# Performance work log

Measured on AMD Instinct MI355X. Metric: run time of the kernel, lower is better.

## Reference

```python
import jax, jax.numpy as jnp
import numpy as np

H, DH = 16, 32  # hardcoded by E's shape [16, seq, 32]


def setup_inputs() -> dict:
    key = jax.random.key(0)
    k1, k2 = jax.random.split(key)
    B, S = 2, 2048
    x = jax.random.normal(k1, (B, S, 3 * H * DH), dtype=jnp.float32)
    E = jax.random.normal(k2, (H, S, DH), dtype=jnp.float32) * 0.02  # learned rel-pos table
    return {"x": x, "E": E}


def _skew(rel):
    # Music-Transformer skew trick: rel [B,H,S,S] -> relative-position alignment.
    B, Hh, S, _ = rel.shape
    rel = jnp.pad(rel, ((0, 0), (0, 0), (0, 0), (1, 0)))  # pad left on last dim
    rel = rel.reshape(B, Hh, S + 1, S)[:, :, 1:]
    return rel


def reference(x, E):
    B, S, _ = x.shape
    q, k, v = jnp.split(x, 3, axis=2)

    def heads(t):
        return t.reshape(B, S, H, DH).transpose(0, 2, 1, 3)  # [B,H,S,DH]

    q, k, v = heads(q), heads(k), heads(v)
    present = jnp.stack([k, v], axis=1)  # [B,2,H,S,DH]

    w = jnp.einsum('bhsd,bhtd->bhst', q, k)            # content scores
    rel = _skew(jnp.einsum('bhsd,hmd->bhsm', q, E))    # relative-position scores
    w = (w + rel) * jax.lax.rsqrt(jnp.float32(DH))     # scale AFTER adding rel (as in source)

    i = jnp.arange(S)[:, None]
    j = jnp.arange(S)[None, :]
    b = (i >= j).astype(w.dtype)                       # causal mask (nd == ns)
    w = w * b - jnp.float32(1e10) * (1.0 - b)
    w = jax.nn.softmax(w, axis=-1)

    a = jnp.einsum('bhst,bhtd->bhsd', w, v)
    a = a.transpose(0, 2, 1, 3).reshape(B, S, H * DH)  # merge heads -> [B,S,512]
    return a, present
```

## Files before the change

kernel.cpp:

```cpp
#include <hip/hip_runtime.h>
#include <hip/hip_bf16.h>

#define NH   16
#define DHD  32
#define SEQ  2048
#define NB   2
#define XROW 1536
#define PP   72

typedef unsigned short u16;
typedef __attribute__((ext_vector_type(8))) short bf16x8;
typedef __attribute__((ext_vector_type(4))) float f32x4;

static __device__ __forceinline__ u16 f2b(float f) {
    __hip_bfloat16 h = __float2bfloat16(f);
    return *(u16*)&h;
}

__global__ __launch_bounds__(256)
void prep_all(const float* __restrict__ x, const float* __restrict__ E,
              u16* __restrict__ Kb, u16* __restrict__ Vt, u16* __restrict__ Eb,
              float* __restrict__ pres) {
    __shared__ float t[64][33];
    int bid = blockIdx.x;
    int tid = threadIdx.x;
    if (bid < 1024) {
        long o = ((long)bid * 256 + tid) * 8;
        int d = (int)(o & 31);
        int s = (int)((o >> 5) & (SEQ - 1));
        int bh = (int)(o >> 16);
        int b = bh >> 4, h = bh & 15;
        const float* src = x + ((long)(b * SEQ + s)) * XROW + 512 + h * 32 + d;
        float4 f0 = *(const float4*)src, f1 = *(const float4*)(src + 4);
        u16 pk[8] = {f2b(f0.x), f2b(f0.y), f2b(f0.z), f2b(f0.w),
                     f2b(f1.x), f2b(f1.y), f2b(f1.z), f2b(f1.w)};
        *(uint4*)(Kb + o) = *(uint4*)pk;
    } else if (bid < 1536) {
        long o = ((long)(bid - 1024) * 256 + tid) * 8;
        const float* src = E + o;
        float4 f0 = *(const float4*)src, f1 = *(const float4*)(src + 4);
        u16 pk[8] = {f2b(f0.x), f2b(f0.y), f2b(f0.z), f2b(f0.w),
                     f2b(f1.x), f2b(f1.y), f2b(f1.z), f2b(f1.w)};
        *(uint4*)(Eb + o) = *(uint4*)pk;
    } else if (bid < 2560) {
        int vb = bid - 1536;
        int bh = vb & 31;
        int s0 = (vb >> 5) << 6;
        int b = bh >> 4, h = bh & 15;
        int sr = tid >> 3, d4 = (tid & 7) * 4;
        const float* base = x + (long)b * SEQ * XROW + 1024 + h * 32;
        float4 f = *(const float4*)(base + (long)(s0 + sr) * XROW + d4);
        t[sr][d4] = f.x; t[sr][d4+1] = f.y; t[sr][d4+2] = f.z; t[sr][d4+3] = f.w;
        f = *(const float4*)(base + (long)(s0 + sr + 32) * XROW + d4);
        t[sr+32][d4] = f.x; t[sr+32][d4+1] = f.y; t[sr+32][d4+2] = f.z; t[sr+32][d4+3] = f.w;
        __syncthreads();
        int d = tid >> 3, sg = (tid & 7) * 8;
        u16 pk[8];
#pragma unroll
        for (int k = 0; k < 8; ++k) pk[k] = f2b(t[sg + k][d]);
        *(uint4*)(Vt + ((long)(bh * 32 + d)) * SEQ + s0 + sg) = *(uint4*)pk;
    } else {
        long o = ((long)(bid - 2560) * 256 + tid) * 4;
        int d0 = (int)(o & 31);
        int s  = (int)((o >> 5) & (SEQ - 1));
        int h  = (int)((o >> 16) & (NH - 1));
        int c  = (int)((o >> 20) & 1);
        int b  = (int)(o >> 21);
        const float4* in = (const float4*)(x + ((long)(b * SEQ + s)) * XROW
                                           + (1 + c) * 512 + h * 32 + d0);
        *((float4*)(pres + o)) = in[0];
    }
}

__global__ __launch_bounds__(256, 8)
void attn_mfma(const float* __restrict__ x, const u16* __restrict__ Kb,
               const u16* __restrict__ Vt, const u16* __restrict__ Eb,
               float* __restrict__ out) {
    __shared__ u16  pls[4][16 * PP];
    __shared__ float comb[4][16][33];

    int bh = blockIdx.x & 31;
    int gt = 127 - (blockIdx.x >> 5);
    int b = bh >> 4, h = bh & 15;
    int wv   = threadIdx.x >> 6;
    int lane = threadIdx.x & 63;
    int n16  = lane & 15;
    int quad = lane >> 4;
    int i0 = gt * 16;

    const u16* Kbh = Kb + (long)bh * SEQ * 32;
    const u16* Vbh = Vt + (long)bh * 32 * SEQ;
    const u16* Ebh = Eb + (long)h * SEQ * 32;

    const float scale = 0.17677669529663687f;
    bf16x8 qf;
    {
        const float* qp = x + ((long)(b * SEQ) + i0 + n16) * XROW + h * 32 + quad * 8;
        float4 f0 = *(const float4*)qp, f1 = *(const float4*)(qp + 4);
        u16 pk[8] = {f2b(f0.x*scale), f2b(f0.y*scale), f2b(f0.z*scale), f2b(f0.w*scale),
                     f2b(f1.x*scale), f2b(f1.y*scale), f2b(f1.z*scale), f2b(f1.w*scale)};
        qf = *(bf16x8*)pk;
    }

    bf16x8 ones;
#pragma unroll
    for (int k = 0; k < 8; ++k) ones[k] = (short)0x3F80;

    f32x4 O0 = {0.f,0.f,0.f,0.f}, O1 = {0.f,0.f,0.f,0.f}, Os = {0.f,0.f,0.f,0.f};
    const f32x4 zero = {0.f,0.f,0.f,0.f};

    u16* pw = &pls[wv][0];
    int cbase = 15 - quad * 4 + n16;
    int permhi = (lane & 48) << 2;

    int nch = (i0 >> 6) + 1;
    for (int ch = wv; ch < nch; ch += 4) {
        int j0c = ch << 6;
        int mw0 = 2032 - i0 + j0c;

        f32x4 P0, P1;
        {
            int row = mw0 + n16; if (row > SEQ - 1) row = SEQ - 1;
            bf16x8 ef = *(const bf16x8*)(Ebh + (long)row * 32 + quad * 8);
            P0 = __builtin_amdgcn_mfma_f32_16x16x32_bf16(qf, ef, zero, 0, 0, 0);
        }
        f32x4 w[4];
#pragma unroll
        for (int s = 0; s < 4; ++s) {
            {
                int row = mw0 + 16 * (s + 1) + n16; if (row > SEQ - 1) row = SEQ - 1;
                bf16x8 ef = *(const bf16x8*)(Ebh + (long)row * 32 + quad * 8);
                P1 = __builtin_amdgcn_mfma_f32_16x16x32_bf16(qf, ef, zero, 0, 0, 0);
            }
            f32x4 C;
            {
                bf16x8 kf = *(const bf16x8*)(Kbh + (long)(j0c + 16*s + n16) * 32 + quad * 8);
                C = __builtin_amdgcn_mfma_f32_16x16x32_bf16(qf, kf, zero, 0, 0, 0);
            }
#pragma unroll
            for (int r = 0; r < 4; ++r) {
                int c = cbase - r;
                int addr = permhi | ((c & 15) << 2);
                int v0 = __builtin_amdgcn_ds_bpermute(addr, __float_as_int(P0[r]));
                int v1 = __builtin_amdgcn_ds_bpermute(addr, __float_as_int(P1[r]));
                float rel = (c < 16) ? __int_as_float(v0) : __int_as_float(v1);
                w[s][r] = C[r] + rel;
            }
            P0 = P1;
        }

        if (ch == nch - 1) {
            int jb = j0c + n16 - i0;
#pragma unroll
            for (int s = 0; s < 4; ++s)
#pragma unroll
                for (int r = 0; r < 4; ++r)
                    if (jb + 16 * s > quad * 4 + r) w[s][r] = -1e30f;
        }

#pragma unroll
        for (int s = 0; s < 4; ++s)
#pragma unroll
            for (int r = 0; r < 4; ++r)
                w[s][r] = __expf(w[s][r]);

#pragma unroll
        for (int s = 0; s < 4; ++s)
#pragma unroll
            for (int r = 0; r < 4; ++r)
                pw[(quad * 4 + r) * PP + 16 * s + n16] = f2b(w[s][r]);

        bf16x8 pa0 = *(const bf16x8*)(pw + n16 * PP + quad * 8);
        bf16x8 pa1 = *(const bf16x8*)(pw + n16 * PP + 32 + quad * 8);

        bf16x8 v00 = *(const bf16x8*)(Vbh + (long)n16 * SEQ        + j0c      + quad * 8);
        bf16x8 v01 = *(const bf16x8*)(Vbh + (long)n16 * SEQ        + j0c + 32 + quad * 8);
        bf16x8 v10 = *(const bf16x8*)(Vbh + (long)(16 + n16) * SEQ + j0c      + quad * 8);
        bf16x8 v11 = *(const bf16x8*)(Vbh + (long)(16 + n16) * SEQ + j0c + 32 + quad * 8);

        O0 = __builtin_amdgcn_mfma_f32_16x16x32_bf16(pa0, v00, O0, 0, 0, 0);
        O0 = __builtin_amdgcn_mfma_f32_16x16x32_bf16(pa1, v01, O0, 0, 0, 0);
        O1 = __builtin_amdgcn_mfma_f32_16x16x32_bf16(pa0, v10, O1, 0, 0, 0);
        O1 = __builtin_amdgcn_mfma_f32_16x16x32_bf16(pa1, v11, O1, 0, 0, 0);
        Os = __builtin_amdgcn_mfma_f32_16x16x32_bf16(pa0, ones, Os, 0, 0, 0);
        Os = __builtin_amdgcn_mfma_f32_16x16x32_bf16(pa1, ones, Os, 0, 0, 0);
    }

#pragma unroll
    for (int r = 0; r < 4; ++r) {
        comb[wv][quad * 4 + r][n16]      = O0[r];
        comb[wv][quad * 4 + r][16 + n16] = O1[r];
        if (n16 == 0) comb[wv][quad * 4 + r][32] = Os[r];
    }
    __syncthreads();

    int row = threadIdx.x >> 4;
    int c2  = (threadIdx.x & 15) * 2;
    float s0 = 0.f, s1 = 0.f, ls = 0.f;
#pragma unroll
    for (int v = 0; v < 4; ++v) {
        s0 += comb[v][row][c2];
        s1 += comb[v][row][c2 + 1];
        ls += comb[v][row][32];
    }
    float inv = 1.0f / ls;
    float* op = out + ((long)(b * SEQ) + i0 + row) * 512 + h * 32 + c2;
    op[0] = s0 * inv;
    op[1] = s1 * inv;
}

__global__ void present_copy(const float* __restrict__ x, float* __restrict__ pres) {
    long o = ((long)blockIdx.x * blockDim.x + threadIdx.x) * 4;
    int d0 = (int)(o & 31);
    int s  = (int)((o >> 5) & (SEQ - 1));
    int h  = (int)((o >> 16) & (NH - 1));
    int c  = (int)((o >> 20) & 1);
    int b  = (int)(o >> 21);
    const float4* in = (const float4*)(x + ((long)(b * SEQ + s)) * XROW
                                       + (1 + c) * 512 + h * 32 + d0);
    *((float4*)(pres + o)) = in[0];
}

__global__ __launch_bounds__(128)
void attn_mono(const float* __restrict__ x, const float* __restrict__ E,
               float* __restrict__ out) {
    __shared__ float kt[64][36];
    __shared__ float vt[64][36];
    __shared__ float et[192][33];
    int bh = blockIdx.x & 31;
    int rt = 15 - (blockIdx.x >> 5);
    int b = bh >> 4, h = bh & 15;
    int tid = threadIdx.x;
    int r0 = rt * 128;
    int i = r0 + tid;
    float q[DHD];
    const float4* q4 = (const float4*)(x + ((long)(b * SEQ + i)) * XROW + h * 32);
#pragma unroll
    for (int t = 0; t < 8; ++t) ((float4*)q)[t] = q4[t];
    float m = -1e30f, l = 0.f;
    float acc[DHD];
#pragma unroll
    for (int d = 0; d < DHD; ++d) acc[d] = 0.f;
    const float* Eh = E + (long)h * SEQ * DHD;
    int ntile = (rt + 1) * 2;
    for (int t0 = 0; t0 < ntile; ++t0) {
        int j0 = t0 * 64;
        {
            int r = tid & 63, isv = tid >> 6;
            const float4* s4 = (const float4*)(x + ((long)(b * SEQ + j0 + r)) * XROW
                                               + (1 + isv) * 512 + h * 32);
            float4 tmp[8];
#pragma unroll
            for (int t = 0; t < 8; ++t) tmp[t] = s4[t];
            float* dst = isv ? &vt[r][0] : &kt[r][0];
#pragma unroll
            for (int t = 0; t < 8; ++t) ((float4*)dst)[t] = tmp[t];
        }
        {
            int eb0 = (SEQ - 1) - (r0 + 127) + j0;
#pragma unroll
            for (int p = 0; p < 12; ++p) {
                int idx = p * 128 + tid;
                int r = idx >> 3, qq = idx & 7;
                int gr = eb0 + r; if (gr > SEQ - 1) gr = SEQ - 1;
                float4 gg = *(const float4*)(Eh + (long)gr * DHD + qq * 4);
                et[r][qq*4+0] = gg.x; et[r][qq*4+1] = gg.y;
                et[r][qq*4+2] = gg.z; et[r][qq*4+3] = gg.w;
            }
        }
        __syncthreads();
        int jend = i - j0 + 1; if (jend > 64) jend = 64;
        int er0 = 127 - tid;
        for (int jj = 0; jj < jend; ++jj) {
            const float* ep = &et[er0 + jj][0];
            float dk = 0.f, de = 0.f;
#pragma unroll
            for (int d = 0; d < DHD; ++d) {
                dk = __builtin_fmaf(q[d], kt[jj][d], dk);
                de = __builtin_fmaf(q[d], ep[d], de);
            }
            float sc = (dk + de) * 0.17677669529663687f;
            if (sc > m) {
                float r = __expf(m - sc);
                l *= r;
#pragma unroll
                for (int d = 0; d < DHD; ++d) acc[d] *= r;
                m = sc;
            }
            float p = __expf(sc - m);
            l += p;
#pragma unroll
            for (int d = 0; d < DHD; ++d)
                acc[d] = __builtin_fmaf(p, vt[jj][d], acc[d]);
        }
        __syncthreads();
    }
    float inv = 1.0f / l;
    float* op = out + ((long)(b * SEQ + i)) * 512 + h * 32;
#pragma unroll
    for (int t = 0; t < 8; ++t) {
        float4 w;
        w.x = acc[t*4+0]*inv; w.y = acc[t*4+1]*inv;
        w.z = acc[t*4+2]*inv; w.w = acc[t*4+3]*inv;
        ((float4*)op)[t] = w;
    }
}

extern "C" void kernel_launch(void* const* d_in, const int* in_sizes, int n_in,
                              void* d_out, int out_size, void* d_ws, size_t ws_size,
                              hipStream_t stream) {
    const float* x = (const float*)d_in[0];
    const float* E = (const float*)d_in[1];
    if (n_in >= 2 && in_sizes[0] == 1048576) { const float* t = x; x = E; E = t; }
    float* a    = (float*)d_out;
    float* pres = a + (long)NB * SEQ * NH * DHD;

    const long KN = (long)NB * NH * SEQ * 32;
    const long EN = (long)NH * SEQ * 32;
    const size_t WS_NEED = (size_t)(2 * KN + EN) * sizeof(u16);
    if (ws_size >= WS_NEED) {
        u16* Kb = (u16*)d_ws;
        u16* Vt = Kb + KN;
        u16* Eb = Vt + KN;
        prep_all<<<dim3(6656), dim3(256), 0, stream>>>(x, E, Kb, Vt, Eb, pres);
        attn_mfma<<<dim3(4096), dim3(256), 0, stream>>>(x, Kb, Vt, Eb, a);
    } else {
        attn_mono<<<dim3(512), dim3(128), 0, stream>>>(x, E, a);
        present_copy<<<dim3(4096), dim3(256), 0, stream>>>(x, pres);
    }
}
```

Before: 154.8 us.

## Fuse present copy into attention kernel and halve rel-pos bpermutes

```diff
diff --git a/kernel.cpp b/kernel.cpp
--- a/kernel.cpp
+++ b/kernel.cpp
@@ -19,8 +19,7 @@
 
 __global__ __launch_bounds__(256)
 void prep_all(const float* __restrict__ x, const float* __restrict__ E,
-              u16* __restrict__ Kb, u16* __restrict__ Vt, u16* __restrict__ Eb,
-              float* __restrict__ pres) {
+              u16* __restrict__ Kb, u16* __restrict__ Vt, u16* __restrict__ Eb) {
     __shared__ float t[64][33];
     int bid = blockIdx.x;
     int tid = threadIdx.x;
@@ -42,7 +41,7 @@
         u16 pk[8] = {f2b(f0.x), f2b(f0.y), f2b(f0.z), f2b(f0.w),
                      f2b(f1.x), f2b(f1.y), f2b(f1.z), f2b(f1.w)};
         *(uint4*)(Eb + o) = *(uint4*)pk;
-    } else if (bid < 2560) {
+    } else {
         int vb = bid - 1536;
         int bh = vb & 31;
         int s0 = (vb >> 5) << 6;
@@ -59,23 +58,13 @@
 #pragma unroll
         for (int k = 0; k < 8; ++k) pk[k] = f2b(t[sg + k][d]);
         *(uint4*)(Vt + ((long)(bh * 32 + d)) * SEQ + s0 + sg) = *(uint4*)pk;
-    } else {
-        long o = ((long)(bid - 2560) * 256 + tid) * 4;
-        int d0 = (int)(o & 31);
-        int s  = (int)((o >> 5) & (SEQ - 1));
-        int h  = (int)((o >> 16) & (NH - 1));
-        int c  = (int)((o >> 20) & 1);
-        int b  = (int)(o >> 21);
-        const float4* in = (const float4*)(x + ((long)(b * SEQ + s)) * XROW
-                                           + (1 + c) * 512 + h * 32 + d0);
-        *((float4*)(pres + o)) = in[0];
     }
 }
 
 __global__ __launch_bounds__(256, 8)
 void attn_mfma(const float* __restrict__ x, const u16* __restrict__ Kb,
                const u16* __restrict__ Vt, const u16* __restrict__ Eb,
-               float* __restrict__ out) {
+               float* __restrict__ out, float* __restrict__ pres) {
     __shared__ u16  pls[4][16 * PP];
     __shared__ float comb[4][16][33];
 
@@ -119,10 +108,17 @@
         int mw0 = 2032 - i0 + j0c;
 
         f32x4 P0, P1;
+        float rel0[4];
         {
             int row = mw0 + n16; if (row > SEQ - 1) row = SEQ - 1;
             bf16x8 ef = *(const bf16x8*)(Ebh + (long)row * 32 + quad * 8);
             P0 = __builtin_amdgcn_mfma_f32_16x16x32_bf16(qf, ef, zero, 0, 0, 0);
+        }
+#pragma unroll
+        for (int r = 0; r < 4; ++r) {
+            int addr = permhi | (((cbase - r) & 15) << 2);
+            rel0[r] = __int_as_float(
+                __builtin_amdgcn_ds_bpermute(addr, __float_as_int(P0[r])));
         }
         f32x4 w[4];
 #pragma unroll
@@ -141,10 +137,11 @@
             for (int r = 0; r < 4; ++r) {
                 int c = cbase - r;
                 int addr = permhi | ((c & 15) << 2);
-                int v0 = __builtin_amdgcn_ds_bpermute(addr, __float_as_int(P0[r]));
-                int v1 = __builtin_amdgcn_ds_bpermute(addr, __float_as_int(P1[r]));
-                float rel = (c < 16) ? __int_as_float(v0) : __int_as_float(v1);
+                float rel1 = __int_as_float(
+                    __builtin_amdgcn_ds_bpermute(addr, __float_as_int(P1[r])));
+                float rel = (c < 16) ? rel0[r] : rel1;
                 w[s][r] = C[r] + rel;
+                rel0[r] = rel1;
             }
             P0 = P1;
         }
@@ -207,6 +204,18 @@
     float* op = out + ((long)(b * SEQ) + i0 + row) * 512 + h * 32 + c2;
     op[0] = s0 * inv;
     op[1] = s1 * inv;
+
+    {
+        long o = ((long)blockIdx.x * 256 + threadIdx.x) * 4;
+        int d0 = (int)(o & 31);
+        int s  = (int)((o >> 5) & (SEQ - 1));
+        int hh = (int)((o >> 16) & (NH - 1));
+        int cc = (int)((o >> 20) & 1);
+        int bb = (int)(o >> 21);
+        const float4* in = (const float4*)(x + ((long)(bb * SEQ + s)) * XROW
+                                           + (1 + cc) * 512 + hh * 32 + d0);
+        *((float4*)(pres + o)) = in[0];
+    }
 }
 
 __global__ void present_copy(const float* __restrict__ x, float* __restrict__ pres) {
@@ -322,8 +331,8 @@
         u16* Kb = (u16*)d_ws;
         u16* Vt = Kb + KN;
         u16* Eb = Vt + KN;
-        prep_all<<<dim3(6656), dim3(256), 0, stream>>>(x, E, Kb, Vt, Eb, pres);
-        attn_mfma<<<dim3(4096), dim3(256), 0, stream>>>(x, Kb, Vt, Eb, a);
+        prep_all<<<dim3(2560), dim3(256), 0, stream>>>(x, E, Kb, Vt, Eb);
+        attn_mfma<<<dim3(4096), dim3(256), 0, stream>>>(x, Kb, Vt, Eb, a, pres);
     } else {
         attn_mono<<<dim3(512), dim3(128), 0, stream>>>(x, E, a);
         present_copy<<<dim3(4096), dim3(256), 0, stream>>>(x, pres);
```

Measured after the change: 149.7 us. 1.03x faster.
